# Performance work log

Hardware: AMD Instinct MI355X
Metric: run time of the kernel (lower is better)

Reference implementation:

```python
import jax, jax.numpy as jnp
import numpy as np

B, S, H = 1, 1024, 2048
NH, HD = 16, 128
E, K, FI, SFI = 8, 2, 1408, 2816
EPS = 1e-6
THETA = 10000.0


def setup_inputs() -> dict:
    key = jax.random.key(0)
    ks = jax.random.split(key, 14)
    sc = 0.02
    return {
        "hidden_states": jax.random.normal(ks[0], (B, S, H), jnp.float32),
        "ln1_w": jnp.ones((H,), jnp.float32),
        "ln2_w": jnp.ones((H,), jnp.float32),
        "wq": jax.random.normal(ks[1], (H, H), jnp.float32) * sc,
        "wk": jax.random.normal(ks[2], (H, H), jnp.float32) * sc,
        "wv": jax.random.normal(ks[3], (H, H), jnp.float32) * sc,
        "wo": jax.random.normal(ks[4], (H, H), jnp.float32) * sc,
        "gate_w": jax.random.normal(ks[5], (E, H), jnp.float32) * sc,
        "expert_gate": jax.random.normal(ks[6], (E, FI, H), jnp.float32) * sc,
        "expert_up": jax.random.normal(ks[7], (E, FI, H), jnp.float32) * sc,
        "expert_down": jax.random.normal(ks[8], (E, H, FI), jnp.float32) * sc,
        "shared_gate": jax.random.normal(ks[9], (SFI, H), jnp.float32) * sc,
        "shared_up": jax.random.normal(ks[10], (SFI, H), jnp.float32) * sc,
        "shared_down": jax.random.normal(ks[11], (H, SFI), jnp.float32) * sc,
    }


def _rmsnorm(x, w):
    v = jnp.mean(x * x, axis=-1, keepdims=True)
    return x * jax.lax.rsqrt(v + EPS) * w


def _rotate_half(x):
    x1, x2 = x[..., : HD // 2], x[..., HD // 2 :]
    return jnp.concatenate((-x2, x1), axis=-1)


def _rope_cos_sin():
    inv_freq = 1.0 / (THETA ** (jnp.arange(0, HD, 2, dtype=jnp.float32) / HD))
    t = jnp.arange(S, dtype=jnp.float32)
    freqs = t[:, None] * inv_freq[None, :]          # [S, HD//2]
    emb = jnp.concatenate((freqs, freqs), axis=-1)  # [S, HD]
    return jnp.cos(emb)[None, None], jnp.sin(emb)[None, None]  # [1,1,S,HD]


def _decoder_layer(hidden_states, ln1_w, ln2_w, wq, wk, wv, wo, gate_w,
                   expert_gate, expert_up, expert_down,
                   shared_gate, shared_up, shared_down):
    # ---- self-attention ----
    residual = hidden_states
    h = _rmsnorm(hidden_states, ln1_w)
    q = (h @ wq.T).reshape(B, S, NH, HD).transpose(0, 2, 1, 3)  # [B,NH,S,HD]
    k = (h @ wk.T).reshape(B, S, NH, HD).transpose(0, 2, 1, 3)
    v = (h @ wv.T).reshape(B, S, NH, HD).transpose(0, 2, 1, 3)
    cos, sin = _rope_cos_sin()
    q = q * cos + _rotate_half(q) * sin
    k = k * cos + _rotate_half(k) * sin
    scores = jnp.einsum('bhqd,bhkd->bhqk', q, k) / jnp.sqrt(jnp.float32(HD))
    causal = jnp.tril(jnp.ones((S, S), bool))
    scores = jnp.where(causal[None, None], scores, jnp.finfo(jnp.float32).min)
    probs = jax.nn.softmax(scores, axis=-1)
    attn = jnp.einsum('bhqk,bhkd->bhqd', probs, v)
    attn = attn.transpose(0, 2, 1, 3).reshape(B, S, H)
    x = residual + attn @ wo.T

    # ---- MoE MLP ----
    residual = x
    h2 = _rmsnorm(x, ln2_w)
    flat = h2.reshape(-1, H)                       # [N,H], N=B*S
    n_tok = flat.shape[0]
    logits = flat @ gate_w.T                       # [N,E]
    gate_scores = jax.nn.softmax(logits, axis=-1)
    topk_w, topk_idx = jax.lax.top_k(gate_scores, K)
    topk_w = topk_w / (jnp.sum(topk_w, axis=-1, keepdims=True) + 1e-20)
    # dense combine weights [N,E] (zero for unrouted experts)
    combine = jnp.zeros((n_tok, E), flat.dtype).at[
        jnp.arange(n_tok)[:, None], topk_idx].add(topk_w)
    # SwiGLU per expert, dense over all experts, then weighted combine
    g = jnp.einsum('nh,efh->enf', flat, expert_gate)   # [E,N,FI]
    u = jnp.einsum('nh,efh->enf', flat, expert_up)
    act = jax.nn.silu(g) * u
    eo = jnp.einsum('enf,ehf->enh', act, expert_down)  # [E,N,H]
    routed = jnp.einsum('enh,ne->nh', eo, combine)
    # shared experts (always on)
    shared = (jax.nn.silu(flat @ shared_gate.T) * (flat @ shared_up.T)) @ shared_down.T
    return residual + (routed + shared).reshape(B, S, H)


def reference(hidden_states, ln1_w, ln2_w, wq, wk, wv, wo, gate_w,
              expert_gate, expert_up, expert_down,
              shared_gate, shared_up, shared_down):
    return _decoder_layer(hidden_states, ln1_w, ln2_w, wq, wk, wv, wo, gate_w,
                          expert_gate, expert_up, expert_down,
                          shared_gate, shared_up, shared_down)
```

## Files before the change

kernel.cpp:

```cpp
#include <hip/hip_runtime.h>
#include <hip/hip_bf16.h>


#define DI __device__ __forceinline__

typedef __attribute__((ext_vector_type(8))) short short8;
typedef __attribute__((ext_vector_type(4))) float f32x4;
using u16 = unsigned short;

struct alignas(8) U16x4 { u16 x, y, z, w; };

DI u16 f2bf(float f) {
  unsigned u = __float_as_uint(f);
  u += 0x7fffu + ((u >> 16) & 1u);
  return (u16)(u >> 16);
}
DI float bf2f(u16 h) { return __uint_as_float(((unsigned)h) << 16); }
DI unsigned pack2(float f0, float f1) {
  unsigned a = __float_as_uint(f0) + 0x8000u;
  unsigned b = __float_as_uint(f1) + 0x8000u;
  return (a >> 16) | (b & 0xffff0000u);
}

DI void gload16(const void* g, void* l) {
  __builtin_amdgcn_global_load_lds((const __attribute__((address_space(1))) void*)g,
                                   (__attribute__((address_space(3))) void*)l, 16, 0, 0);
}


__global__ __launch_bounds__(256) void k_ropetab(float* __restrict__ tab) {
  int idx = blockIdx.x * 256 + threadIdx.x;
  int s = idx >> 6, i = idx & 63;
  double inv = pow(10000.0, -(double)(2 * i) / 128.0);
  double ang = (double)s * inv;
  tab[idx * 2 + 0] = (float)cos(ang);
  tab[idx * 2 + 1] = (float)sin(ang);
}

__global__ __launch_bounds__(256) void k_rmsnorm(const float* __restrict__ in,
                                                 const float* __restrict__ w,
                                                 float* __restrict__ outf,
                                                 u16* __restrict__ outh,
                                                 u16* __restrict__ outl) {
  const int row = blockIdx.x, t = threadIdx.x;
  const float* x = in + (size_t)row * 2048;
  float4 a = *(const float4*)&x[t * 4];
  float4 b = *(const float4*)&x[1024 + t * 4];
  float ss = a.x * a.x + a.y * a.y + a.z * a.z + a.w * a.w +
             b.x * b.x + b.y * b.y + b.z * b.z + b.w * b.w;
#pragma unroll
  for (int off = 32; off; off >>= 1) ss += __shfl_xor(ss, off);
  __shared__ float red[4];
  if ((t & 63) == 0) red[t >> 6] = ss;
  __syncthreads();
  float total = red[0] + red[1] + red[2] + red[3];
  float r = 1.0f / sqrtf(total * (1.0f / 2048.0f) + 1e-6f);
  float4 wa = *(const float4*)&w[t * 4];
  float4 wb = *(const float4*)&w[1024 + t * 4];
  float va[8] = {a.x * r * wa.x, a.y * r * wa.y, a.z * r * wa.z, a.w * r * wa.w,
                 b.x * r * wb.x, b.y * r * wb.y, b.z * r * wb.z, b.w * r * wb.w};
  if (outf) {
    *(float4*)&outf[(size_t)row * 2048 + t * 4] = make_float4(va[0], va[1], va[2], va[3]);
    *(float4*)&outf[(size_t)row * 2048 + 1024 + t * 4] = make_float4(va[4], va[5], va[6], va[7]);
  }
  if (outh) {
    U16x4 ha{f2bf(va[0]), f2bf(va[1]), f2bf(va[2]), f2bf(va[3])};
    U16x4 hb{f2bf(va[4]), f2bf(va[5]), f2bf(va[6]), f2bf(va[7])};
    *(U16x4*)&outh[(size_t)row * 2048 + t * 4] = ha;
    *(U16x4*)&outh[(size_t)row * 2048 + 1024 + t * 4] = hb;
    if (outl) {
      U16x4 la{f2bf(va[0] - bf2f(ha.x)), f2bf(va[1] - bf2f(ha.y)),
               f2bf(va[2] - bf2f(ha.z)), f2bf(va[3] - bf2f(ha.w))};
      U16x4 lb{f2bf(va[4] - bf2f(hb.x)), f2bf(va[5] - bf2f(hb.y)),
               f2bf(va[6] - bf2f(hb.z)), f2bf(va[7] - bf2f(hb.w))};
      *(U16x4*)&outl[(size_t)row * 2048 + t * 4] = la;
      *(U16x4*)&outl[(size_t)row * 2048 + 1024 + t * 4] = lb;
    }
  }
}

__global__ __launch_bounds__(256) void k_splitf4(
    const float* __restrict__ s0, const float* __restrict__ s1,
    const float* __restrict__ s2, const float* __restrict__ s3,
    u16* __restrict__ h0, u16* __restrict__ h1, u16* __restrict__ h2,
    u16* __restrict__ h3, u16* __restrict__ l0, u16* __restrict__ l1,
    u16* __restrict__ l2, u16* __restrict__ l3) {
  const int which = blockIdx.x >> 12;
  const int idx = ((blockIdx.x & 4095) * 256 + threadIdx.x) * 4;
  const float* src = (which == 0) ? s0 : (which == 1) ? s1 : (which == 2) ? s2 : s3;
  u16* dh = (which == 0) ? h0 : (which == 1) ? h1 : (which == 2) ? h2 : h3;
  u16* dl = (which == 0) ? l0 : (which == 1) ? l1 : (which == 2) ? l2 : l3;
  float4 v = *(const float4*)&src[idx];
  U16x4 h{f2bf(v.x), f2bf(v.y), f2bf(v.z), f2bf(v.w)};
  U16x4 l{f2bf(v.x - bf2f(h.x)), f2bf(v.y - bf2f(h.y)),
          f2bf(v.z - bf2f(h.z)), f2bf(v.w - bf2f(h.w))};
  *(U16x4*)&dh[idx] = h;
  *(U16x4*)&dl[idx] = l;
}

__global__ __launch_bounds__(256) void k_rope(float* __restrict__ q, float* __restrict__ k,
                                              const float* __restrict__ tab) {
  int idx = blockIdx.x * 256 + threadIdx.x;
  int s = idx >> 10, rem = idx & 1023;
  int h = rem >> 6, i = rem & 63;
  size_t base = (size_t)s * 2048 + h * 128 + i;
  float c = tab[(s * 64 + i) * 2 + 0];
  float sn = tab[(s * 64 + i) * 2 + 1];
  const float qs = 0.08838834764831845f;
  float q1 = q[base], q2 = q[base + 64];
  q[base] = (q1 * c - q2 * sn) * qs;
  q[base + 64] = (q2 * c + q1 * sn) * qs;
  float k1 = k[base], k2 = k[base + 64];
  k[base] = k1 * c - k2 * sn;
  k[base + 64] = k2 * c + k1 * sn;
}

__global__ __launch_bounds__(256) void k_splitkv(
    const float* __restrict__ qf, const float* __restrict__ kf,
    const float* __restrict__ vf,
    u16* __restrict__ Qh, u16* __restrict__ Ql,
    u16* __restrict__ Kh, u16* __restrict__ Kl,
    u16* __restrict__ Vth, u16* __restrict__ Vtl) {
  int idx = (blockIdx.x * 256 + threadIdx.x) * 4;
  int s = idx >> 11, c = idx & 2047;
  float4 q4 = *(const float4*)&qf[idx];
  U16x4 qh{f2bf(q4.x), f2bf(q4.y), f2bf(q4.z), f2bf(q4.w)};
  U16x4 ql{f2bf(q4.x - bf2f(qh.x)), f2bf(q4.y - bf2f(qh.y)),
           f2bf(q4.z - bf2f(qh.z)), f2bf(q4.w - bf2f(qh.w))};
  *(U16x4*)&Qh[idx] = qh; *(U16x4*)&Ql[idx] = ql;
  float4 k4 = *(const float4*)&kf[idx];
  U16x4 kh{f2bf(k4.x), f2bf(k4.y), f2bf(k4.z), f2bf(k4.w)};
  U16x4 kl{f2bf(k4.x - bf2f(kh.x)), f2bf(k4.y - bf2f(kh.y)),
           f2bf(k4.z - bf2f(kh.z)), f2bf(k4.w - bf2f(kh.w))};
  *(U16x4*)&Kh[idx] = kh; *(U16x4*)&Kl[idx] = kl;
  float4 v4 = *(const float4*)&vf[idx];
  float vv[4] = {v4.x, v4.y, v4.z, v4.w};
#pragma unroll
  for (int i = 0; i < 4; ++i) {
    u16 hv = f2bf(vv[i]);
    u16 lv = f2bf(vv[i] - bf2f(hv));
    Vth[(size_t)(c + i) * 1024 + s] = hv;
    Vtl[(size_t)(c + i) * 1024 + s] = lv;
  }
}

DI void stage_kv(const u16* __restrict__ Khg, const u16* __restrict__ Klg,
                 const u16* __restrict__ Vhg, const u16* __restrict__ Vlg,
                 u16* lsKh, u16* lsKl, u16* lsVh, u16* lsVl,
                 int kvb, int hh, int wv, int lane) {
#pragma unroll
  for (int it = 0; it < 4; ++it) {
    const int ebase = it * 2048 + wv * 512;
    const int eo = ebase + lane * 8;
    {
      const int rr = eo >> 7, cg = (eo >> 3) & 15;
      const size_t src = (size_t)(kvb + rr) * 2048 + hh * 128 + ((cg ^ (rr & 7)) << 3);
      gload16(Khg + src, lsKh + ebase);
      gload16(Klg + src, lsKl + ebase);
    }
    {
      const int rr = eo >> 6, cg = (eo >> 3) & 7;
      const size_t src = (size_t)(hh * 128 + rr) * 1024 + kvb + ((cg ^ (rr & 7)) << 3);
      gload16(Vhg + src, lsVh + ebase);
      gload16(Vlg + src, lsVl + ebase);
    }
  }
}

__global__ __launch_bounds__(256) void k_attn_tile(
    const u16* __restrict__ Qh, const u16* __restrict__ Ql,
    const u16* __restrict__ Khg, const u16* __restrict__ Klg,
    const u16* __restrict__ Vhg, const u16* __restrict__ Vlg,
    u16* __restrict__ atth, u16* __restrict__ attl) {
  __shared__ u16 lsKh[2][8192], lsKl[2][8192], lsVh[2][8192], lsVl[2][8192];
  __shared__ u16 Plh[4][16][72], Pll[4][16][72];
  const int hh = blockIdx.y;
  const int qb = blockIdx.x * 64;
  const int tid = threadIdx.x, lane = tid & 63, wv = tid >> 6;
  const int l15 = lane & 15, grp = lane >> 4;
  u16(*plh)[72] = Plh[wv];
  u16(*pll)[72] = Pll[wv];
  const int q_glob = qb + wv * 16 + l15;
  const int tend = blockIdx.x + 1;

  short8 qfh[4], qfl[4];
  const size_t qbase = (size_t)q_glob * 2048 + hh * 128;
#pragma unroll
  for (int c = 0; c < 4; ++c) {
    qfh[c] = *(const short8*)&Qh[qbase + c * 32 + grp * 8];
    qfl[c] = *(const short8*)&Ql[qbase + c * 32 + grp * 8];
  }
  f32x4 oacc[8];
#pragma unroll
  for (int dc = 0; dc < 8; ++dc) oacc[dc] = 0.f;
  float m_run = -1e30f, l_run = 0.f;

  int cur = 0;
  stage_kv(Khg, Klg, Vhg, Vlg, lsKh[0], lsKl[0], lsVh[0], lsVl[0], 0, hh, wv, lane);
  __syncthreads();

  for (int kt = 0; kt < tend; ++kt) {
    const int kvb = kt * 64;
    if (kt + 1 < tend)
      stage_kv(Khg, Klg, Vhg, Vlg, lsKh[cur ^ 1], lsKl[cur ^ 1], lsVh[cur ^ 1],
               lsVl[cur ^ 1], kvb + 64, hh, wv, lane);
    const u16* kh = lsKh[cur];
    const u16* kl = lsKl[cur];
    const u16* vh = lsVh[cur];
    const u16* vl = lsVl[cur];

    f32x4 s4[4];
#pragma unroll
    for (int sub = 0; sub < 4; ++sub) {
      f32x4 a = {0.f, 0.f, 0.f, 0.f};
      const int kr = sub * 16 + l15;
      const int sw = kr & 7;
#pragma unroll
      for (int c = 0; c < 4; ++c) {
        const int off = kr * 128 + ((((c << 2) | grp) ^ sw) << 3);
        short8 khf = *(const short8*)&kh[off];
        short8 klf = *(const short8*)&kl[off];
        a = __builtin_amdgcn_mfma_f32_16x16x32_bf16(khf, qfh[c], a, 0, 0, 0);
        a = __builtin_amdgcn_mfma_f32_16x16x32_bf16(klf, qfh[c], a, 0, 0, 0);
        a = __builtin_amdgcn_mfma_f32_16x16x32_bf16(khf, qfl[c], a, 0, 0, 0);
      }
      s4[sub] = a;
    }
    if (kt == tend - 1) {
#pragma unroll
      for (int sub = 0; sub < 4; ++sub)
#pragma unroll
        for (int r = 0; r < 4; ++r) {
          int kv = kvb + sub * 16 + grp * 4 + r;
          if (kv > q_glob) s4[sub][r] = -1e30f;
        }
    }
    float tmax = s4[0][0];
#pragma unroll
    for (int sub = 0; sub < 4; ++sub)
#pragma unroll
      for (int r = 0; r < 4; ++r) tmax = fmaxf(tmax, s4[sub][r]);
    tmax = fmaxf(tmax, __shfl_xor(tmax, 16));
    tmax = fmaxf(tmax, __shfl_xor(tmax, 32));
    float mnew = fmaxf(m_run, tmax);
    float scale = expf(m_run - mnew);
    float p[16], lsum = 0.f;
#pragma unroll
    for (int sub = 0; sub < 4; ++sub)
#pragma unroll
      for (int r = 0; r < 4; ++r) {
        float pe = expf(s4[sub][r] - mnew);
        p[sub * 4 + r] = pe;
        lsum += pe;
      }
    lsum += __shfl_xor(lsum, 16);
    lsum += __shfl_xor(lsum, 32);
    l_run = l_run * scale + lsum;
    m_run = mnew;
#pragma unroll
    for (int dc = 0; dc < 8; ++dc) oacc[dc] *= scale;
#pragma unroll
    for (int sub = 0; sub < 4; ++sub)
#pragma unroll
      for (int rp = 0; rp < 2; ++rp) {
        int i0 = sub * 4 + rp * 2;
        u16 h0 = f2bf(p[i0]), h1 = f2bf(p[i0 + 1]);
        u16 lo0 = f2bf(p[i0] - bf2f(h0)), lo1 = f2bf(p[i0 + 1] - bf2f(h1));
        int kvoff = sub * 16 + grp * 4 + rp * 2;
        *(unsigned*)&plh[l15][kvoff] = (unsigned)h0 | ((unsigned)h1 << 16);
        *(unsigned*)&pll[l15][kvoff] = (unsigned)lo0 | ((unsigned)lo1 << 16);
      }
    short8 phf[2], plf[2];
#pragma unroll
    for (int ks = 0; ks < 2; ++ks) {
      phf[ks] = *(const short8*)&plh[l15][ks * 32 + grp * 8];
      plf[ks] = *(const short8*)&pll[l15][ks * 32 + grp * 8];
    }
#pragma unroll
    for (int dc = 0; dc < 8; ++dc) {
      const int dr = dc * 16 + l15;
      const int sw = dr & 7;
      f32x4 acc = oacc[dc];
#pragma unroll
      for (int ks = 0; ks < 2; ++ks) {
        const int voff = dr * 64 + ((((ks << 2) | grp) ^ sw) << 3);
        short8 vhf = *(const short8*)&vh[voff];
        short8 vlf = *(const short8*)&vl[voff];
        acc = __builtin_amdgcn_mfma_f32_16x16x32_bf16(vhf, phf[ks], acc, 0, 0, 0);
        acc = __builtin_amdgcn_mfma_f32_16x16x32_bf16(vlf, phf[ks], acc, 0, 0, 0);
        acc = __builtin_amdgcn_mfma_f32_16x16x32_bf16(vhf, plf[ks], acc, 0, 0, 0);
      }
      oacc[dc] = acc;
    }
    __syncthreads();
    cur ^= 1;
  }
  float inv = 1.0f / l_run;
#pragma unroll
  for (int dc = 0; dc < 8; ++dc)
#pragma unroll
    for (int rp = 0; rp < 2; ++rp) {
      float v0 = oacc[dc][rp * 2] * inv;
      float v1 = oacc[dc][rp * 2 + 1] * inv;
      u16 h0 = f2bf(v0), h1 = f2bf(v1);
      u16 lo0 = f2bf(v0 - bf2f(h0)), lo1 = f2bf(v1 - bf2f(h1));
      size_t o = (size_t)q_glob * 2048 + hh * 128 + dc * 16 + grp * 4 + rp * 2;
      *(unsigned*)&atth[o] = (unsigned)h0 | ((unsigned)h1 << 16);
      *(unsigned*)&attl[o] = (unsigned)lo0 | ((unsigned)lo1 << 16);
    }
}

__global__ __launch_bounds__(256) void k_router(const float* __restrict__ h2f,
                                                const float* __restrict__ gw,
                                                int2* __restrict__ tidx,
                                                float2* __restrict__ twgt) {
  const int tok = blockIdx.x;
  const float* hrow = h2f + (size_t)tok * 2048;
  float part[8];
#pragma unroll
  for (int e = 0; e < 8; ++e) part[e] = 0.f;
  for (int j = 0; j < 8; ++j) {
    int p = j * 256 + threadIdx.x;
    float hv = hrow[p];
#pragma unroll
    for (int e = 0; e < 8; ++e) part[e] += hv * gw[e * 2048 + p];
  }
#pragma unroll
  for (int e = 0; e < 8; ++e)
#pragma unroll
    for (int off = 32; off; off >>= 1) part[e] += __shfl_xor(part[e], off);
  __shared__ float red[4][8];
  int wv = threadIdx.x >> 6, lane = threadIdx.x & 63;
  if (lane == 0) {
#pragma unroll
    for (int e = 0; e < 8; ++e) red[wv][e] = part[e];
  }
  __syncthreads();
  if (threadIdx.x == 0) {
    float lg[8];
#pragma unroll
    for (int e = 0; e < 8; ++e) lg[e] = red[0][e] + red[1][e] + red[2][e] + red[3][e];
    float m = lg[0];
#pragma unroll
    for (int e = 1; e < 8; ++e) m = fmaxf(m, lg[e]);
    float ex[8], s = 0.f;
#pragma unroll
    for (int e = 0; e < 8; ++e) { ex[e] = expf(lg[e] - m); s += ex[e]; }
#pragma unroll
    for (int e = 0; e < 8; ++e) ex[e] /= s;
    int i1 = 0;
#pragma unroll
    for (int e = 1; e < 8; ++e) if (ex[e] > ex[i1]) i1 = e;
    int i2 = (i1 == 0) ? 1 : 0;
#pragma unroll
    for (int e = 0; e < 8; ++e) if (e != i1 && ex[e] > ex[i2]) i2 = e;
    float s2 = ex[i1] + ex[i2] + 1e-20f;
    tidx[tok] = make_int2(i1, i2);
    twgt[tok] = make_float2(ex[i1] / s2, ex[i2] / s2);
  }
}

__global__ __launch_bounds__(64) void k_scan(const int2* __restrict__ tidx,
                                             const float2* __restrict__ twgt,
                                             int* __restrict__ meta,
                                             int* __restrict__ toklist,
                                             float* __restrict__ slotw,
                                             int* __restrict__ slots) {
  const int lane = threadIdx.x;
  int base = 0;
  for (int e = 0; e < 8; ++e) {
    int cnt = 0;
    for (int c = 0; c < 16; ++c) {
      const int tok = c * 64 + lane;
      int2 my = tidx[tok];
      int f1 = (my.x == e), f2 = (my.y == e);
      int flag = f1 | f2;
      unsigned long long m = __ballot(flag);
      if (flag) {
        float2 w = twgt[tok];
        int rank = (int)__popcll(m & ((1ull << lane) - 1ull));
        int s = base + cnt + rank;
        toklist[s] = tok;
        slotw[s] = f1 ? w.x : w.y;
        slots[tok * 2 + (f1 ? 0 : 1)] = s;
      }
      cnt += (int)__popcll(m);
    }
    if (lane == 0) { meta[e] = base; meta[9 + e] = cnt; }
    const int padded = ((cnt + 127) >> 7) << 7;
    for (int s = cnt + lane; s < padded; s += 64) {
      toklist[base + s] = 0;
      slotw[base + s] = 0.f;
    }
    base += padded;
  }
  if (lane == 0) meta[8] = base;
}


DI void stageA_bf16(const u16* __restrict__ A, size_t lda, int row0, int k0,
                    u16* lsA, int tid) {
  const int lane = tid & 63, wv = tid >> 6;
#pragma unroll
  for (int it = 0; it < 2; ++it) {
    const int ebase = it * 2048 + wv * 512;
    const int eo = ebase + lane * 8;
    const int rr = eo >> 5, cc = eo & 31;
    gload16(A + (size_t)(row0 + rr) * lda + k0 + cc, lsA + ebase);
  }
}

__global__ __launch_bounds__(256) void k_gemm_bf16split(
    const u16* __restrict__ Ah, const u16* __restrict__ Al,
    const u16* __restrict__ Bh0, const u16* __restrict__ Bl0,
    const u16* __restrict__ Bh1, const u16* __restrict__ Bl1,
    const u16* __restrict__ Bh2, const u16* __restrict__ Bl2,
    float* __restrict__ C0, float* __restrict__ C1, float* __restrict__ C2,
    const float* __restrict__ resid) {
  __shared__ u16 lsAh[4096], lsAl[4096], lsBh[4096], lsBl[4096];
  const int z = blockIdx.z;
  const u16* Bh = (z == 0) ? Bh0 : (z == 1) ? Bh1 : Bh2;
  const u16* Bl = (z == 0) ? Bl0 : (z == 1) ? Bl1 : Bl2;
  float* Cm = (z == 0) ? C0 : (z == 1) ? C1 : C2;
  const int tid = threadIdx.x, lane = tid & 63, wv = tid >> 6;
  const int wr = (wv >> 1) * 64, wc = (wv & 1) * 64;
  const int fr = lane & 15, fg = lane >> 4;
  const int row0 = blockIdx.x * 128, col0 = blockIdx.y * 128;
  f32x4 acc[4][4];
#pragma unroll
  for (int i = 0; i < 4; ++i)
#pragma unroll
    for (int j = 0; j < 4; ++j) acc[i][j] = 0.f;

  for (int kt = 0; kt < 64; ++kt) {
    const int k0 = kt * 32;
    stageA_bf16(Ah, 2048, row0, k0, lsAh, tid);
    stageA_bf16(Al, 2048, row0, k0, lsAl, tid);
    stageA_bf16(Bh, 2048, col0, k0, lsBh, tid);
    stageA_bf16(Bl, 2048, col0, k0, lsBl, tid);
    __syncthreads();
    short8 ah[4], al[4], bh[4], bl[4];
#pragma unroll
    for (int mi = 0; mi < 4; ++mi) {
      const int off = (wr + mi * 16 + fr) * 32 + fg * 8;
      ah[mi] = *(const short8*)&lsAh[off];
      al[mi] = *(const short8*)&lsAl[off];
    }
#pragma unroll
    for (int ni = 0; ni < 4; ++ni) {
      const int off = (wc + ni * 16 + fr) * 32 + fg * 8;
      bh[ni] = *(const short8*)&lsBh[off];
      bl[ni] = *(const short8*)&lsBl[off];
    }
#pragma unroll
    for (int mi = 0; mi < 4; ++mi)
#pragma unroll
      for (int ni = 0; ni < 4; ++ni) {
        f32x4 c = acc[mi][ni];
        c = __builtin_amdgcn_mfma_f32_16x16x32_bf16(al[mi], bh[ni], c, 0, 0, 0);
        c = __builtin_amdgcn_mfma_f32_16x16x32_bf16(ah[mi], bl[ni], c, 0, 0, 0);
        c = __builtin_amdgcn_mfma_f32_16x16x32_bf16(ah[mi], bh[ni], c, 0, 0, 0);
        acc[mi][ni] = c;
      }
    __syncthreads();
  }
  const bool hasres = (resid != nullptr);
#pragma unroll
  for (int mi = 0; mi < 4; ++mi)
#pragma unroll
    for (int ni = 0; ni < 4; ++ni)
#pragma unroll
      for (int qq = 0; qq < 4; ++qq) {
        const int row = row0 + wr + mi * 16 + fg * 4 + qq;
        const int col = col0 + wc + ni * 16 + fr;
        float val = acc[mi][ni][qq];
        if (hasres) val += resid[(size_t)row * 2048 + col];
        Cm[(size_t)row * 2048 + col] = val;
      }
}

DI int tile_to_expert(const int* meta, int t) {
  int e = 0;
  while (e < 7 && t >= (meta[e + 1] >> 7)) ++e;
  return e;
}

__global__ __launch_bounds__(256) void k_dual_all(
    const u16* __restrict__ h2b, const float* __restrict__ eg,
    const float* __restrict__ eu, const float* __restrict__ sg,
    const float* __restrict__ su, const int* __restrict__ meta,
    const int* __restrict__ toklist, const float* __restrict__ slotw,
    u16* __restrict__ act, u16* __restrict__ acts) {
  const int wid = blockIdx.x;
  const bool isShared = wid >= 528;
  __shared__ int toks[128];
  __shared__ u16 lsA[2][4096], lsG[2][2048], lsU[2][2048];
  const int tid = threadIdx.x, lane = tid & 63, wv = tid >> 6;
  const int wr = (wv >> 1) * 64, wc = (wv & 1) * 32;
  const int fr = lane & 15, fg = lane >> 4;

  int n0, off_e = 0, cnt_e = 0, rtile = 0;
  const float *Bg, *Bu;
  if (isShared) {
    const int b2 = wid - 528;
    rtile = b2 / 44;
    n0 = (b2 % 44) * 64;
    Bg = sg;
    Bu = su;
    if (tid < 128) toks[tid] = rtile * 128 + tid;
  } else {
    const int t = wid / 22;
    if (t >= (meta[8] >> 7)) return;
    n0 = (wid % 22) * 64;
    const int e = tile_to_expert(meta, t);
    off_e = meta[e];
    cnt_e = meta[9 + e];
    rtile = t - (off_e >> 7);
    Bg = eg + (size_t)e * 1408 * 2048;
    Bu = eu + (size_t)e * 1408 * 2048;
    if (tid < 128) toks[tid] = toklist[off_e + rtile * 128 + tid] & 1023;
  }
  f32x4 ag[4][2], au[4][2];
#pragma unroll
  for (int i = 0; i < 4; ++i)
#pragma unroll
    for (int j = 0; j < 2; ++j) { ag[i][j] = 0.f; au[i][j] = 0.f; }
  __syncthreads();

  const int ebase0 = wv * 512, ebase1 = 2048 + wv * 512;
  const int eoA0 = ebase0 + lane * 8, eoA1 = ebase1 + lane * 8;
  const u16* aS0 = h2b + (size_t)toks[eoA0 >> 5] * 2048 + (eoA0 & 31);
  const u16* aS1 = h2b + (size_t)toks[eoA1 >> 5] * 2048 + (eoA1 & 31);
  const int eoB0 = tid * 4, eoB1 = (256 + tid) * 4;
  const float* gB0 = Bg + (size_t)(n0 + (eoB0 >> 5)) * 2048 + (eoB0 & 31);
  const float* gB1 = Bg + (size_t)(n0 + (eoB1 >> 5)) * 2048 + (eoB1 & 31);
  const float* uB0 = Bu + (size_t)(n0 + (eoB0 >> 5)) * 2048 + (eoB0 & 31);
  const float* uB1 = Bu + (size_t)(n0 + (eoB1 >> 5)) * 2048 + (eoB1 & 31);

  float4 g0, g1, u0, u1;
  gload16(aS0, lsA[0] + ebase0);
  gload16(aS1, lsA[0] + ebase1);
  g0 = *(const float4*)gB0; g1 = *(const float4*)gB1;
  u0 = *(const float4*)uB0; u1 = *(const float4*)uB1;
  *(unsigned*)&lsG[0][eoB0] = pack2(g0.x, g0.y);
  *(unsigned*)&lsG[0][eoB0 + 2] = pack2(g0.z, g0.w);
  *(unsigned*)&lsG[0][eoB1] = pack2(g1.x, g1.y);
  *(unsigned*)&lsG[0][eoB1 + 2] = pack2(g1.z, g1.w);
  *(unsigned*)&lsU[0][eoB0] = pack2(u0.x, u0.y);
  *(unsigned*)&lsU[0][eoB0 + 2] = pack2(u0.z, u0.w);
  *(unsigned*)&lsU[0][eoB1] = pack2(u1.x, u1.y);
  *(unsigned*)&lsU[0][eoB1 + 2] = pack2(u1.z, u1.w);
  __syncthreads();

  int cur = 0;
  for (int kt = 0; kt < 64; ++kt) {
    const int k1 = (kt + 1) * 32;
    const bool pf = (kt + 1 < 64);
    if (pf) {
      gload16(aS0 + k1, lsA[cur ^ 1] + ebase0);
      gload16(aS1 + k1, lsA[cur ^ 1] + ebase1);
      g0 = *(const float4*)(gB0 + k1);
      g1 = *(const float4*)(gB1 + k1);
      u0 = *(const float4*)(uB0 + k1);
      u1 = *(const float4*)(uB1 + k1);
    }
    short8 af[4], gf[2], uf[2];
#pragma unroll
    for (int mi = 0; mi < 4; ++mi)
      af[mi] = *(const short8*)&lsA[cur][(wr + mi * 16 + fr) * 32 + fg * 8];
#pragma unroll
    for (int ni = 0; ni < 2; ++ni) {
      const int off = (wc + ni * 16 + fr) * 32 + fg * 8;
      gf[ni] = *(const short8*)&lsG[cur][off];
      uf[ni] = *(const short8*)&lsU[cur][off];
    }
#pragma unroll
    for (int mi = 0; mi < 4; ++mi)
#pragma unroll
      for (int ni = 0; ni < 2; ++ni) {
        ag[mi][ni] = __builtin_amdgcn_mfma_f32_16x16x32_bf16(af[mi], gf[ni], ag[mi][ni], 0, 0, 0);
        au[mi][ni] = __builtin_amdgcn_mfma_f32_16x16x32_bf16(af[mi], uf[ni], au[mi][ni], 0, 0, 0);
      }
    if (pf) {
      u16* lg = lsG[cur ^ 1];
      u16* lu = lsU[cur ^ 1];
      *(unsigned*)&lg[eoB0] = pack2(g0.x, g0.y);
      *(unsigned*)&lg[eoB0 + 2] = pack2(g0.z, g0.w);
      *(unsigned*)&lg[eoB1] = pack2(g1.x, g1.y);
      *(unsigned*)&lg[eoB1 + 2] = pack2(g1.z, g1.w);
      *(unsigned*)&lu[eoB0] = pack2(u0.x, u0.y);
      *(unsigned*)&lu[eoB0 + 2] = pack2(u0.z, u0.w);
      *(unsigned*)&lu[eoB1] = pack2(u1.x, u1.y);
      *(unsigned*)&lu[eoB1 + 2] = pack2(u1.z, u1.w);
    }
    __syncthreads();
    cur ^= 1;
  }
#pragma unroll
  for (int mi = 0; mi < 4; ++mi)
#pragma unroll
    for (int ni = 0; ni < 2; ++ni)
#pragma unroll
      for (int qq = 0; qq < 4; ++qq) {
        const int r = wr + mi * 16 + fg * 4 + qq;
        const int col = n0 + wc + ni * 16 + fr;
        float g = ag[mi][ni][qq], u = au[mi][ni][qq];
        float a = g / (1.0f + expf(-g)) * u;
        if (isShared) {
          acts[(size_t)(rtile * 128 + r) * 2816 + col] = f2bf(a);
        } else {
          const int rowInE = rtile * 128 + r;
          if (rowInE < cnt_e)
            act[(size_t)(off_e + rowInE) * 1408 + col] = f2bf(a * slotw[off_e + rowInE]);
        }
      }
}

__global__ __launch_bounds__(256) void k_down_all(
    const u16* __restrict__ act, const float* __restrict__ ed,
    const u16* __restrict__ acts, const float* __restrict__ sd,
    const int* __restrict__ meta, float* __restrict__ dwn,
    float* __restrict__ shd) {
  __shared__ u16 lsA[2][4096], lsB[2][4096];
  const int wid = blockIdx.x;
  const int tid = threadIdx.x, lane = tid & 63, wv = tid >> 6;
  const int fr = lane & 15, fg = lane >> 4;
  const int ebase0 = wv * 512, ebase1 = 2048 + wv * 512;
  const int eoA0 = ebase0 + lane * 8, eoA1 = ebase1 + lane * 8;
  if (wid < 384) {
    const int t = wid >> 4;
    if (t >= (meta[8] >> 7)) return;
    const int col0 = (wid & 15) * 128;
    const int e = tile_to_expert(meta, t);
    const int off_e = meta[e];
    const int rtile = t - (off_e >> 7);
    const int wr = (wv >> 1) * 64, wc = (wv & 1) * 64;
    const u16* Ab = act + (size_t)off_e * 1408;
    const float* Bb = ed + (size_t)e * 2048 * 1408;
    const u16* aS0 = Ab + (size_t)(rtile * 128 + (eoA0 >> 5)) * 1408 + (eoA0 & 31);
    const u16* aS1 = Ab + (size_t)(rtile * 128 + (eoA1 >> 5)) * 1408 + (eoA1 & 31);
    const float* bB[4];
    int eoB[4];
#pragma unroll
    for (int j = 0; j < 4; ++j) {
      eoB[j] = (j * 256 + tid) * 4;
      bB[j] = Bb + (size_t)(col0 + (eoB[j] >> 5)) * 1408 + (eoB[j] & 31);
    }
    f32x4 acc[4][4];
#pragma unroll
    for (int i = 0; i < 4; ++i)
#pragma unroll
      for (int j = 0; j < 4; ++j) acc[i][j] = 0.f;
    float4 bp[4];
    gload16(aS0, lsA[0] + ebase0);
    gload16(aS1, lsA[0] + ebase1);
#pragma unroll
    for (int j = 0; j < 4; ++j) bp[j] = *(const float4*)bB[j];
#pragma unroll
    for (int j = 0; j < 4; ++j) {
      *(unsigned*)&lsB[0][eoB[j]] = pack2(bp[j].x, bp[j].y);
      *(unsigned*)&lsB[0][eoB[j] + 2] = pack2(bp[j].z, bp[j].w);
    }
    __syncthreads();
    int cur = 0;
    for (int kt = 0; kt < 44; ++kt) {
      const int k1 = (kt + 1) * 32;
      const bool pf = (kt + 1 < 44);
      if (pf) {
        gload16(aS0 + k1, lsA[cur ^ 1] + ebase0);
        gload16(aS1 + k1, lsA[cur ^ 1] + ebase1);
#pragma unroll
        for (int j = 0; j < 4; ++j) bp[j] = *(const float4*)(bB[j] + k1);
      }
      short8 af[4], bf_[4];
#pragma unroll
      for (int mi = 0; mi < 4; ++mi)
        af[mi] = *(const short8*)&lsA[cur][(wr + mi * 16 + fr) * 32 + fg * 8];
#pragma unroll
      for (int ni = 0; ni < 4; ++ni)
        bf_[ni] = *(const short8*)&lsB[cur][(wc + ni * 16 + fr) * 32 + fg * 8];
#pragma unroll
      for (int mi = 0; mi < 4; ++mi)
#pragma unroll
        for (int ni = 0; ni < 4; ++ni)
          acc[mi][ni] = __builtin_amdgcn_mfma_f32_16x16x32_bf16(af[mi], bf_[ni], acc[mi][ni], 0, 0, 0);
      if (pf) {
        u16* lb = lsB[cur ^ 1];
#pragma unroll
        for (int j = 0; j < 4; ++j) {
          *(unsigned*)&lb[eoB[j]] = pack2(bp[j].x, bp[j].y);
          *(unsigned*)&lb[eoB[j] + 2] = pack2(bp[j].z, bp[j].w);
        }
      }
      __syncthreads();
      cur ^= 1;
    }
#pragma unroll
    for (int mi = 0; mi < 4; ++mi)
#pragma unroll
      for (int ni = 0; ni < 4; ++ni)
#pragma unroll
        for (int qq = 0; qq < 4; ++qq) {
          const int r = wr + mi * 16 + fg * 4 + qq;
          const int col = col0 + wc + ni * 16 + fr;
          dwn[(size_t)(off_e + rtile * 128 + r) * 2048 + col] = acc[mi][ni][qq];
        }
  } else {
    const int b2 = wid - 384;
    const int row0 = (b2 >> 5) * 128;
    const int col0 = (b2 & 31) * 64;
    const int wr = (wv >> 1) * 64, wc = (wv & 1) * 32;
    const u16* aS0 = acts + (size_t)(row0 + (eoA0 >> 5)) * 2816 + (eoA0 & 31);
    const u16* aS1 = acts + (size_t)(row0 + (eoA1 >> 5)) * 2816 + (eoA1 & 31);
    const float* bB[2];
    int eoB[2];
#pragma unroll
    for (int j = 0; j < 2; ++j) {
      eoB[j] = (j * 256 + tid) * 4;
      bB[j] = sd + (size_t)(col0 + (eoB[j] >> 5)) * 2816 + (eoB[j] & 31);
    }
    f32x4 acc[4][2];
#pragma unroll
    for (int i = 0; i < 4; ++i)
#pragma unroll
      for (int j = 0; j < 2; ++j) acc[i][j] = 0.f;
    float4 bp[2];
    gload16(aS0, lsA[0] + ebase0);
    gload16(aS1, lsA[0] + ebase1);
#pragma unroll
    for (int j = 0; j < 2; ++j) bp[j] = *(const float4*)bB[j];
#pragma unroll
    for (int j = 0; j < 2; ++j) {
      *(unsigned*)&lsB[0][eoB[j]] = pack2(bp[j].x, bp[j].y);
      *(unsigned*)&lsB[0][eoB[j] + 2] = pack2(bp[j].z, bp[j].w);
    }
    __syncthreads();
    int cur = 0;
    for (int kt = 0; kt < 88; ++kt) {
      const int k1 = (kt + 1) * 32;
      const bool pf = (kt + 1 < 88);
      if (pf) {
        gload16(aS0 + k1, lsA[cur ^ 1] + ebase0);
        gload16(aS1 + k1, lsA[cur ^ 1] + ebase1);
#pragma unroll
        for (int j = 0; j < 2; ++j) bp[j] = *(const float4*)(bB[j] + k1);
      }
      short8 af[4], bf_[2];
#pragma unroll
      for (int mi = 0; mi < 4; ++mi)
        af[mi] = *(const short8*)&lsA[cur][(wr + mi * 16 + fr) * 32 + fg * 8];
#pragma unroll
      for (int ni = 0; ni < 2; ++ni)
        bf_[ni] = *(const short8*)&lsB[cur][(wc + ni * 16 + fr) * 32 + fg * 8];
#pragma unroll
      for (int mi = 0; mi < 4; ++mi)
#pragma unroll
        for (int ni = 0; ni < 2; ++ni)
          acc[mi][ni] = __builtin_amdgcn_mfma_f32_16x16x32_bf16(af[mi], bf_[ni], acc[mi][ni], 0, 0, 0);
      if (pf) {
        u16* lb = lsB[cur ^ 1];
#pragma unroll
        for (int j = 0; j < 2; ++j) {
          *(unsigned*)&lb[eoB[j]] = pack2(bp[j].x, bp[j].y);
          *(unsigned*)&lb[eoB[j] + 2] = pack2(bp[j].z, bp[j].w);
        }
      }
      __syncthreads();
      cur ^= 1;
    }
#pragma unroll
    for (int mi = 0; mi < 4; ++mi)
#pragma unroll
      for (int ni = 0; ni < 2; ++ni)
#pragma unroll
        for (int qq = 0; qq < 4; ++qq) {
          const int row = row0 + wr + mi * 16 + fg * 4 + qq;
          const int col = col0 + wc + ni * 16 + fr;
          shd[(size_t)row * 2048 + col] = acc[mi][ni][qq];
        }
  }
}

__global__ __launch_bounds__(256) void k_combine(
    const float* __restrict__ shd, const float* __restrict__ x,
    const float* __restrict__ dwn, const int* __restrict__ slots,
    float* __restrict__ outp) {
  const int i4 = (blockIdx.x * 256 + threadIdx.x) * 4;
  const int row = i4 >> 11, col = i4 & 2047;
  const int s0 = slots[row * 2], s1 = slots[row * 2 + 1];
  float4 a = *(const float4*)&shd[i4];
  float4 b = *(const float4*)&x[i4];
  float4 c = *(const float4*)&dwn[(size_t)s0 * 2048 + col];
  float4 d = *(const float4*)&dwn[(size_t)s1 * 2048 + col];
  float4 o;
  o.x = a.x + b.x + c.x + d.x;
  o.y = a.y + b.y + c.y + d.y;
  o.z = a.z + b.z + c.z + d.z;
  o.w = a.w + b.w + c.w + d.w;
  *(float4*)&outp[i4] = o;
}


extern "C" void kernel_launch(void* const* d_in, const int* in_sizes, int n_in,
                              void* d_out, int out_size, void* d_ws, size_t ws_size,
                              hipStream_t stream) {
  (void)in_sizes; (void)n_in; (void)out_size; (void)ws_size;
  const float* hidden = (const float*)d_in[0];
  const float* ln1 = (const float*)d_in[1];
  const float* ln2 = (const float*)d_in[2];
  const float* wq = (const float*)d_in[3];
  const float* wk = (const float*)d_in[4];
  const float* wvw = (const float*)d_in[5];
  const float* wo = (const float*)d_in[6];
  const float* gw = (const float*)d_in[7];
  const float* eg = (const float*)d_in[8];
  const float* eu = (const float*)d_in[9];
  const float* ed = (const float*)d_in[10];
  const float* sg = (const float*)d_in[11];
  const float* su = (const float*)d_in[12];
  const float* sd = (const float*)d_in[13];
  float* out = (float*)d_out;
  char* ws = (char*)d_ws;

  const size_t KB = 1ull << 10, MB = 1ull << 20;
  float* tab = (float*)(ws + 0);
  int2* tidx = (int2*)(ws + 512 * KB);
  float2* twgt = (float2*)(ws + 520 * KB);
  int* meta = (int*)(ws + 528 * KB);
  int* tokl = (int*)(ws + 532 * KB);
  float* slw = (float*)(ws + 544 * KB);
  int* slots = (int*)(ws + 556 * KB);
  u16* hnh = (u16*)(ws + 1 * MB);
  u16* hnl = (u16*)(ws + 5 * MB);
  u16* wqh = (u16*)(ws + 9 * MB);
  u16* wql = (u16*)(ws + 17 * MB);
  u16* wkh = (u16*)(ws + 25 * MB);
  u16* wkl = (u16*)(ws + 33 * MB);
  u16* wvh = (u16*)(ws + 41 * MB);
  u16* wvl = (u16*)(ws + 49 * MB);
  u16* woh = (u16*)(ws + 57 * MB);
  u16* wol = (u16*)(ws + 65 * MB);
  float* qf = (float*)(ws + 73 * MB);
  float* kf = (float*)(ws + 81 * MB);
  float* vf = (float*)(ws + 89 * MB);
  u16* Qh = (u16*)(ws + 9 * MB);
  u16* Ql = (u16*)(ws + 13 * MB);
  u16* Kh = (u16*)(ws + 17 * MB);
  u16* Kl = (u16*)(ws + 21 * MB);
  u16* Vth = (u16*)(ws + 25 * MB);
  u16* Vtl = (u16*)(ws + 29 * MB);
  u16* atth = (u16*)(ws + 33 * MB);
  u16* attl = (u16*)(ws + 37 * MB);
  float* xf = (float*)(ws + 41 * MB);
  float* h2f = (float*)(ws + 49 * MB);
  u16* h2b = (u16*)(ws + 1 * MB);
  u16* act = (u16*)(ws + 73 * MB);
  u16* acts = (u16*)(ws + 82 * MB);
  float* dwn = (float*)(ws + 9 * MB);
  float* shd = (float*)(ws + 33 * MB);

  k_ropetab<<<256, 256, 0, stream>>>(tab);
  k_rmsnorm<<<1024, 256, 0, stream>>>(hidden, ln1, nullptr, hnh, hnl);
  k_splitf4<<<16384, 256, 0, stream>>>(wq, wk, wvw, wo, wqh, wkh, wvh, woh,
                                       wql, wkl, wvl, wol);
  k_gemm_bf16split<<<dim3(8, 16, 3), 256, 0, stream>>>(
      hnh, hnl, wqh, wql, wkh, wkl, wvh, wvl, qf, kf, vf, nullptr);
  k_rope<<<4096, 256, 0, stream>>>(qf, kf, tab);
  k_splitkv<<<2048, 256, 0, stream>>>(qf, kf, vf, Qh, Ql, Kh, Kl, Vth, Vtl);
  k_attn_tile<<<dim3(16, 16), 256, 0, stream>>>(Qh, Ql, Kh, Kl, Vth, Vtl, atth, attl);
  k_gemm_bf16split<<<dim3(8, 16, 1), 256, 0, stream>>>(
      atth, attl, woh, wol, woh, wol, woh, wol, xf, xf, xf, hidden);
  k_rmsnorm<<<1024, 256, 0, stream>>>(xf, ln2, h2f, h2b, nullptr);
  k_router<<<1024, 256, 0, stream>>>(h2f, gw, tidx, twgt);
  k_scan<<<1, 64, 0, stream>>>(tidx, twgt, meta, tokl, slw, slots);
  k_dual_all<<<880, 256, 0, stream>>>(h2b, eg, eu, sg, su, meta, tokl, slw, act, acts);
  k_down_all<<<640, 256, 0, stream>>>(act, ed, acts, sd, meta, dwn, shd);
  k_combine<<<2048, 256, 0, stream>>>(shd, xf, dwn, slots, out);
}
```

Before: 582.7 us.

## Deepen MoE GEMM pipelines to prefetch two k-tiles ahead with partial waits

```diff
diff --git a/kernel.cpp b/kernel.cpp
--- a/kernel.cpp
+++ b/kernel.cpp
@@ -494,7 +494,7 @@
   const int wid = blockIdx.x;
   const bool isShared = wid >= 528;
   __shared__ int toks[128];
-  __shared__ u16 lsA[2][4096], lsG[2][2048], lsU[2][2048];
+  __shared__ u16 lsA[3][4096], lsG[2][2048], lsU[2][2048];
   const int tid = threadIdx.x, lane = tid & 63, wv = tid >> 6;
   const int wr = (wv >> 1) * 64, wc = (wv & 1) * 32;
   const int fr = lane & 15, fg = lane >> 4;
@@ -537,42 +537,55 @@
   const float* uB0 = Bu + (size_t)(n0 + (eoB0 >> 5)) * 2048 + (eoB0 & 31);
   const float* uB1 = Bu + (size_t)(n0 + (eoB1 >> 5)) * 2048 + (eoB1 & 31);
 
-  float4 g0, g1, u0, u1;
-  gload16(aS0, lsA[0] + ebase0);
-  gload16(aS1, lsA[0] + ebase1);
-  g0 = *(const float4*)gB0; g1 = *(const float4*)gB1;
-  u0 = *(const float4*)uB0; u1 = *(const float4*)uB1;
-  *(unsigned*)&lsG[0][eoB0] = pack2(g0.x, g0.y);
-  *(unsigned*)&lsG[0][eoB0 + 2] = pack2(g0.z, g0.w);
-  *(unsigned*)&lsG[0][eoB1] = pack2(g1.x, g1.y);
-  *(unsigned*)&lsG[0][eoB1 + 2] = pack2(g1.z, g1.w);
-  *(unsigned*)&lsU[0][eoB0] = pack2(u0.x, u0.y);
-  *(unsigned*)&lsU[0][eoB0 + 2] = pack2(u0.z, u0.w);
-  *(unsigned*)&lsU[0][eoB1] = pack2(u1.x, u1.y);
-  *(unsigned*)&lsU[0][eoB1 + 2] = pack2(u1.z, u1.w);
-  __syncthreads();
-
-  int cur = 0;
-  for (int kt = 0; kt < 64; ++kt) {
-    const int k1 = (kt + 1) * 32;
-    const bool pf = (kt + 1 < 64);
-    if (pf) {
-      gload16(aS0 + k1, lsA[cur ^ 1] + ebase0);
-      gload16(aS1 + k1, lsA[cur ^ 1] + ebase1);
-      g0 = *(const float4*)(gB0 + k1);
-      g1 = *(const float4*)(gB1 + k1);
-      u0 = *(const float4*)(uB0 + k1);
-      u1 = *(const float4*)(uB1 + k1);
-    }
+  u16 *pA0 = lsA[0], *pA1 = lsA[1], *pA2 = lsA[2];
+  float4 gX0, gX1, uX0, uX1, gY0, gY1, uY0, uY1;
+
+  gload16(aS0, pA0 + ebase0);
+  gload16(aS1, pA0 + ebase1);
+  gX0 = *(const float4*)gB0; gX1 = *(const float4*)gB1;
+  uX0 = *(const float4*)uB0; uX1 = *(const float4*)uB1;
+  gload16(aS0 + 32, pA1 + ebase0);
+  gload16(aS1 + 32, pA1 + ebase1);
+  gY0 = *(const float4*)(gB0 + 32); gY1 = *(const float4*)(gB1 + 32);
+  uY0 = *(const float4*)(uB0 + 32); uY1 = *(const float4*)(uB1 + 32);
+  {
+    u16* lg = lsG[0];
+    u16* lu = lsU[0];
+    *(unsigned*)&lg[eoB0] = pack2(gX0.x, gX0.y);
+    *(unsigned*)&lg[eoB0 + 2] = pack2(gX0.z, gX0.w);
+    *(unsigned*)&lg[eoB1] = pack2(gX1.x, gX1.y);
+    *(unsigned*)&lg[eoB1 + 2] = pack2(gX1.z, gX1.w);
+    *(unsigned*)&lu[eoB0] = pack2(uX0.x, uX0.y);
+    *(unsigned*)&lu[eoB0 + 2] = pack2(uX0.z, uX0.w);
+    *(unsigned*)&lu[eoB1] = pack2(uX1.x, uX1.y);
+    *(unsigned*)&lu[eoB1 + 2] = pack2(uX1.z, uX1.w);
+  }
+  asm volatile("s_waitcnt vmcnt(6) lgkmcnt(0)" ::: "memory");
+  __builtin_amdgcn_s_barrier();
+  asm volatile("" ::: "memory");
+
+  auto iter = [&](int k, float4& Wg0, float4& Wg1, float4& Wu0, float4& Wu1,
+                  float4& Lg0, float4& Lg1, float4& Lu0, float4& Lu1) {
+    if (k + 2 < 64) {
+      const int k2 = (k + 2) * 32;
+      gload16(aS0 + k2, pA2 + ebase0);
+      gload16(aS1 + k2, pA2 + ebase1);
+      Lg0 = *(const float4*)(gB0 + k2);
+      Lg1 = *(const float4*)(gB1 + k2);
+      Lu0 = *(const float4*)(uB0 + k2);
+      Lu1 = *(const float4*)(uB1 + k2);
+    }
+    const u16* lgc = lsG[k & 1];
+    const u16* luc = lsU[k & 1];
     short8 af[4], gf[2], uf[2];
 #pragma unroll
     for (int mi = 0; mi < 4; ++mi)
-      af[mi] = *(const short8*)&lsA[cur][(wr + mi * 16 + fr) * 32 + fg * 8];
+      af[mi] = *(const short8*)&pA0[(wr + mi * 16 + fr) * 32 + fg * 8];
 #pragma unroll
     for (int ni = 0; ni < 2; ++ni) {
       const int off = (wc + ni * 16 + fr) * 32 + fg * 8;
-      gf[ni] = *(const short8*)&lsG[cur][off];
-      uf[ni] = *(const short8*)&lsU[cur][off];
+      gf[ni] = *(const short8*)&lgc[off];
+      uf[ni] = *(const short8*)&luc[off];
     }
 #pragma unroll
     for (int mi = 0; mi < 4; ++mi)
@@ -581,21 +594,32 @@
         ag[mi][ni] = __builtin_amdgcn_mfma_f32_16x16x32_bf16(af[mi], gf[ni], ag[mi][ni], 0, 0, 0);
         au[mi][ni] = __builtin_amdgcn_mfma_f32_16x16x32_bf16(af[mi], uf[ni], au[mi][ni], 0, 0, 0);
       }
-    if (pf) {
-      u16* lg = lsG[cur ^ 1];
-      u16* lu = lsU[cur ^ 1];
-      *(unsigned*)&lg[eoB0] = pack2(g0.x, g0.y);
-      *(unsigned*)&lg[eoB0 + 2] = pack2(g0.z, g0.w);
-      *(unsigned*)&lg[eoB1] = pack2(g1.x, g1.y);
-      *(unsigned*)&lg[eoB1 + 2] = pack2(g1.z, g1.w);
-      *(unsigned*)&lu[eoB0] = pack2(u0.x, u0.y);
-      *(unsigned*)&lu[eoB0 + 2] = pack2(u0.z, u0.w);
-      *(unsigned*)&lu[eoB1] = pack2(u1.x, u1.y);
-      *(unsigned*)&lu[eoB1 + 2] = pack2(u1.z, u1.w);
-    }
-    __syncthreads();
-    cur ^= 1;
-  }
+    if (k < 63) {
+      u16* lg = lsG[(k + 1) & 1];
+      u16* lu = lsU[(k + 1) & 1];
+      *(unsigned*)&lg[eoB0] = pack2(Wg0.x, Wg0.y);
+      *(unsigned*)&lg[eoB0 + 2] = pack2(Wg0.z, Wg0.w);
+      *(unsigned*)&lg[eoB1] = pack2(Wg1.x, Wg1.y);
+      *(unsigned*)&lg[eoB1 + 2] = pack2(Wg1.z, Wg1.w);
+      *(unsigned*)&lu[eoB0] = pack2(Wu0.x, Wu0.y);
+      *(unsigned*)&lu[eoB0 + 2] = pack2(Wu0.z, Wu0.w);
+      *(unsigned*)&lu[eoB1] = pack2(Wu1.x, Wu1.y);
+      *(unsigned*)&lu[eoB1 + 2] = pack2(Wu1.z, Wu1.w);
+    }
+    if (k < 62)
+      asm volatile("s_waitcnt vmcnt(6) lgkmcnt(0)" ::: "memory");
+    else
+      asm volatile("s_waitcnt vmcnt(0) lgkmcnt(0)" ::: "memory");
+    __builtin_amdgcn_s_barrier();
+    asm volatile("" ::: "memory");
+    u16* t = pA0; pA0 = pA1; pA1 = pA2; pA2 = t;
+  };
+
+  for (int kt = 0; kt < 64; kt += 2) {
+    iter(kt, gY0, gY1, uY0, uY1, gX0, gX1, uX0, uX1);
+    iter(kt + 1, gX0, gX1, uX0, uX1, gY0, gY1, uY0, uY1);
+  }
+
 #pragma unroll
   for (int mi = 0; mi < 4; ++mi)
 #pragma unroll
@@ -621,12 +645,14 @@
     const u16* __restrict__ acts, const float* __restrict__ sd,
     const int* __restrict__ meta, float* __restrict__ dwn,
     float* __restrict__ shd) {
-  __shared__ u16 lsA[2][4096], lsB[2][4096];
+  __shared__ u16 lsA[3][4096], lsB[2][4096];
   const int wid = blockIdx.x;
   const int tid = threadIdx.x, lane = tid & 63, wv = tid >> 6;
   const int fr = lane & 15, fg = lane >> 4;
   const int ebase0 = wv * 512, ebase1 = 2048 + wv * 512;
   const int eoA0 = ebase0 + lane * 8, eoA1 = ebase1 + lane * 8;
+  u16 *pA0 = lsA[0], *pA1 = lsA[1], *pA2 = lsA[2];
+
   if (wid < 384) {
     const int t = wid >> 4;
     if (t >= (meta[8] >> 7)) return;
@@ -651,49 +677,64 @@
     for (int i = 0; i < 4; ++i)
 #pragma unroll
       for (int j = 0; j < 4; ++j) acc[i][j] = 0.f;
-    float4 bp[4];
-    gload16(aS0, lsA[0] + ebase0);
-    gload16(aS1, lsA[0] + ebase1);
-#pragma unroll
-    for (int j = 0; j < 4; ++j) bp[j] = *(const float4*)bB[j];
+    float4 bX[4], bY[4];
+    gload16(aS0, pA0 + ebase0);
+    gload16(aS1, pA0 + ebase1);
+#pragma unroll
+    for (int j = 0; j < 4; ++j) bX[j] = *(const float4*)bB[j];
+    gload16(aS0 + 32, pA1 + ebase0);
+    gload16(aS1 + 32, pA1 + ebase1);
+#pragma unroll
+    for (int j = 0; j < 4; ++j) bY[j] = *(const float4*)(bB[j] + 32);
 #pragma unroll
     for (int j = 0; j < 4; ++j) {
-      *(unsigned*)&lsB[0][eoB[j]] = pack2(bp[j].x, bp[j].y);
-      *(unsigned*)&lsB[0][eoB[j] + 2] = pack2(bp[j].z, bp[j].w);
-    }
-    __syncthreads();
-    int cur = 0;
-    for (int kt = 0; kt < 44; ++kt) {
-      const int k1 = (kt + 1) * 32;
-      const bool pf = (kt + 1 < 44);
-      if (pf) {
-        gload16(aS0 + k1, lsA[cur ^ 1] + ebase0);
-        gload16(aS1 + k1, lsA[cur ^ 1] + ebase1);
-#pragma unroll
-        for (int j = 0; j < 4; ++j) bp[j] = *(const float4*)(bB[j] + k1);
-      }
+      *(unsigned*)&lsB[0][eoB[j]] = pack2(bX[j].x, bX[j].y);
+      *(unsigned*)&lsB[0][eoB[j] + 2] = pack2(bX[j].z, bX[j].w);
+    }
+    asm volatile("s_waitcnt vmcnt(6) lgkmcnt(0)" ::: "memory");
+    __builtin_amdgcn_s_barrier();
+    asm volatile("" ::: "memory");
+
+    auto iter = [&](int k, float4 (&W)[4], float4 (&L)[4]) {
+      if (k + 2 < 44) {
+        const int k2 = (k + 2) * 32;
+        gload16(aS0 + k2, pA2 + ebase0);
+        gload16(aS1 + k2, pA2 + ebase1);
+#pragma unroll
+        for (int j = 0; j < 4; ++j) L[j] = *(const float4*)(bB[j] + k2);
+      }
+      const u16* lbc = lsB[k & 1];
       short8 af[4], bf_[4];
 #pragma unroll
       for (int mi = 0; mi < 4; ++mi)
-        af[mi] = *(const short8*)&lsA[cur][(wr + mi * 16 + fr) * 32 + fg * 8];
+        af[mi] = *(const short8*)&pA0[(wr + mi * 16 + fr) * 32 + fg * 8];
 #pragma unroll
       for (int ni = 0; ni < 4; ++ni)
-        bf_[ni] = *(const short8*)&lsB[cur][(wc + ni * 16 + fr) * 32 + fg * 8];
+        bf_[ni] = *(const short8*)&lbc[(wc + ni * 16 + fr) * 32 + fg * 8];
 #pragma unroll
       for (int mi = 0; mi < 4; ++mi)
 #pragma unroll
         for (int ni = 0; ni < 4; ++ni)
           acc[mi][ni] = __builtin_amdgcn_mfma_f32_16x16x32_bf16(af[mi], bf_[ni], acc[mi][ni], 0, 0, 0);
-      if (pf) {
-        u16* lb = lsB[cur ^ 1];
+      if (k < 43) {
+        u16* lb = lsB[(k + 1) & 1];
 #pragma unroll
         for (int j = 0; j < 4; ++j) {
-          *(unsigned*)&lb[eoB[j]] = pack2(bp[j].x, bp[j].y);
-          *(unsigned*)&lb[eoB[j] + 2] = pack2(bp[j].z, bp[j].w);
+          *(unsigned*)&lb[eoB[j]] = pack2(W[j].x, W[j].y);
+          *(unsigned*)&lb[eoB[j] + 2] = pack2(W[j].z, W[j].w);
         }
       }
-      __syncthreads();
-      cur ^= 1;
+      if (k < 42)
+        asm volatile("s_waitcnt vmcnt(6) lgkmcnt(0)" ::: "memory");
+      else
+        asm volatile("s_waitcnt vmcnt(0) lgkmcnt(0)" ::: "memory");
+      __builtin_amdgcn_s_barrier();
+      asm volatile("" ::: "memory");
+      u16* t2 = pA0; pA0 = pA1; pA1 = pA2; pA2 = t2;
+    };
+    for (int kt = 0; kt < 44; kt += 2) {
+      iter(kt, bY, bX);
+      iter(kt + 1, bX, bY);
     }
 #pragma unroll
     for (int mi = 0; mi < 4; ++mi)
@@ -724,49 +765,64 @@
     for (int i = 0; i < 4; ++i)
 #pragma unroll
       for (int j = 0; j < 2; ++j) acc[i][j] = 0.f;
-    float4 bp[2];
-    gload16(aS0, lsA[0] + ebase0);
-    gload16(aS1, lsA[0] + ebase1);
-#pragma unroll
-    for (int j = 0; j < 2; ++j) bp[j] = *(const float4*)bB[j];
+    float4 cX[2], cY[2];
+    gload16(aS0, pA0 + ebase0);
+    gload16(aS1, pA0 + ebase1);
+#pragma unroll
+    for (int j = 0; j < 2; ++j) cX[j] = *(const float4*)bB[j];
+    gload16(aS0 + 32, pA1 + ebase0);
+    gload16(aS1 + 32, pA1 + ebase1);
+#pragma unroll
+    for (int j = 0; j < 2; ++j) cY[j] = *(const float4*)(bB[j] + 32);
 #pragma unroll
     for (int j = 0; j < 2; ++j) {
-      *(unsigned*)&lsB[0][eoB[j]] = pack2(bp[j].x, bp[j].y);
-      *(unsigned*)&lsB[0][eoB[j] + 2] = pack2(bp[j].z, bp[j].w);
-    }
-    __syncthreads();
-    int cur = 0;
-    for (int kt = 0; kt < 88; ++kt) {
-      const int k1 = (kt + 1) * 32;
-      const bool pf = (kt + 1 < 88);
-      if (pf) {
-        gload16(aS0 + k1, lsA[cur ^ 1] + ebase0);
-        gload16(aS1 + k1, lsA[cur ^ 1] + ebase1);
-#pragma unroll
-        for (int j = 0; j < 2; ++j) bp[j] = *(const float4*)(bB[j] + k1);
-      }
+      *(unsigned*)&lsB[0][eoB[j]] = pack2(cX[j].x, cX[j].y);
+      *(unsigned*)&lsB[0][eoB[j] + 2] = pack2(cX[j].z, cX[j].w);
+    }
+    asm volatile("s_waitcnt vmcnt(4) lgkmcnt(0)" ::: "memory");
+    __builtin_amdgcn_s_barrier();
+    asm volatile("" ::: "memory");
+
+    auto iter = [&](int k, float4 (&W)[2], float4 (&L)[2]) {
+      if (k + 2 < 88) {
+        const int k2 = (k + 2) * 32;
+        gload16(aS0 + k2, pA2 + ebase0);
+        gload16(aS1 + k2, pA2 + ebase1);
+#pragma unroll
+        for (int j = 0; j < 2; ++j) L[j] = *(const float4*)(bB[j] + k2);
+      }
+      const u16* lbc = lsB[k & 1];
       short8 af[4], bf_[2];
 #pragma unroll
       for (int mi = 0; mi < 4; ++mi)
-        af[mi] = *(const short8*)&lsA[cur][(wr + mi * 16 + fr) * 32 + fg * 8];
+        af[mi] = *(const short8*)&pA0[(wr + mi * 16 + fr) * 32 + fg * 8];
 #pragma unroll
       for (int ni = 0; ni < 2; ++ni)
-        bf_[ni] = *(const short8*)&lsB[cur][(wc + ni * 16 + fr) * 32 + fg * 8];
+        bf_[ni] = *(const short8*)&lbc[(wc + ni * 16 + fr) * 32 + fg * 8];
 #pragma unroll
       for (int mi = 0; mi < 4; ++mi)
 #pragma unroll
         for (int ni = 0; ni < 2; ++ni)
           acc[mi][ni] = __builtin_amdgcn_mfma_f32_16x16x32_bf16(af[mi], bf_[ni], acc[mi][ni], 0, 0, 0);
-      if (pf) {
-        u16* lb = lsB[cur ^ 1];
+      if (k < 87) {
+        u16* lb = lsB[(k + 1) & 1];
 #pragma unroll
         for (int j = 0; j < 2; ++j) {
-          *(unsigned*)&lb[eoB[j]] = pack2(bp[j].x, bp[j].y);
-          *(unsigned*)&lb[eoB[j] + 2] = pack2(bp[j].z, bp[j].w);
+          *(unsigned*)&lb[eoB[j]] = pack2(W[j].x, W[j].y);
+          *(unsigned*)&lb[eoB[j] + 2] = pack2(W[j].z, W[j].w);
         }
       }
-      __syncthreads();
-      cur ^= 1;
+      if (k < 86)
+        asm volatile("s_waitcnt vmcnt(4) lgkmcnt(0)" ::: "memory");
+      else
+        asm volatile("s_waitcnt vmcnt(0) lgkmcnt(0)" ::: "memory");
+      __builtin_amdgcn_s_barrier();
+      asm volatile("" ::: "memory");
+      u16* t2 = pA0; pA0 = pA1; pA1 = pA2; pA2 = t2;
+    };
+    for (int kt = 0; kt < 88; kt += 2) {
+      iter(kt, cY, cX);
+      iter(kt + 1, cX, cY);
     }
 #pragma unroll
     for (int mi = 0; mi < 4; ++mi)
```

Result: slower. 644.0 us (+10.5%).
